# Kernel optimization log

Hardware: AMD Instinct MI355X
Metric: run time of the kernel (lower is better)

## Reference

```python
import jax, jax.numpy as jnp
import numpy as np

GROUP_SIZE = 16
MIN_SIGMA = 1e-4


def setup_inputs() -> dict:
    key = jax.random.key(0)
    k1, k2, k3 = jax.random.split(key, 3)
    B, N, M, F = 4, 8192, 4096, 64
    return {
        "point_cloud": jax.random.normal(k1, (B, 3, N), dtype=jnp.float32),
        "query_cloud": jax.random.normal(k2, (B, 3, M), dtype=jnp.float32),
        "point_features": jax.random.normal(k3, (B, F, N), dtype=jnp.float32),
        "temperature": jnp.asarray(1.0, dtype=jnp.float32),
    }


def reference(point_cloud, query_cloud, point_features, temperature):
    # point_cloud: (B,3,N), query_cloud: (B,3,M), point_features: (B,F,N)
    k = GROUP_SIZE
    # Pairwise squared distances (B, M, N): ||q||^2 + ||p||^2 - 2 q.p
    q_sq = jnp.sum(query_cloud ** 2, axis=1)              # (B, M)
    p_sq = jnp.sum(point_cloud ** 2, axis=1)              # (B, N)
    qp = jnp.einsum('bdm,bdn->bmn', query_cloud, point_cloud)
    d2 = q_sq[:, :, None] + p_sq[:, None, :] - 2.0 * qp   # (B, M, N)
    # k nearest neighbors per query
    _, idx = jax.lax.top_k(-d2, k)                         # (B, M, k)

    # Gather neighbor coords and features: (B, 3, M, k), (B, F, M, k)
    idx_b = idx[:, None, :, :]                             # (B,1,M,k)
    grouped_points = jnp.take_along_axis(
        point_cloud[:, :, None, :], jnp.broadcast_to(idx_b, (idx.shape[0], 3, idx.shape[1], k)), axis=3)
    grouped_features = jnp.take_along_axis(
        point_features[:, :, None, :],
        jnp.broadcast_to(idx_b, (idx.shape[0], point_features.shape[1], idx.shape[1], k)), axis=3)

    # Soft-projection weights
    sigma = jnp.maximum(temperature ** 2, jnp.asarray(MIN_SIGMA, dtype=temperature.dtype))
    deltas = grouped_points - query_cloud[:, :, :, None]   # (B,3,M,k)
    dist = jnp.sum(deltas ** 2, axis=1, keepdims=True) / sigma  # (B,1,M,k)
    weights = jax.nn.softmax(-dist, axis=3)                # (B,1,M,k)

    projected_points = jnp.sum(grouped_points * weights, axis=3)     # (B,3,M)
    propagated_features = jnp.sum(grouped_features * weights, axis=3)  # (B,F,M)
    return (projected_points, propagated_features)
```

## Files before the change

kernel.cpp:

```cpp
#include <hip/hip_runtime.h>


#define BB 4
#define NN 8192
#define MM 4096
#define FF 64
#define KK 16
#define CHUNK 2048
#define NCHUNK 4
#define QPW 8
#define QPB 64
#define SCAP 54
#define NTHR 1024

__global__ __launch_bounds__(256) void transpose_feat(const float* __restrict__ pf,
                                                      float* __restrict__ pfT) {
    __shared__ float tile[64][65];
    const int b = blockIdx.y;
    const int n0 = blockIdx.x * 64;
    const int t = threadIdx.x;
    const int n = t & 63, fq = t >> 6;
#pragma unroll
    for (int i = 0; i < 16; ++i) {
        int f = fq * 16 + i;
        tile[f][n] = pf[(size_t)b * FF * NN + (size_t)f * NN + n0 + n];
    }
    __syncthreads();
    const int f2 = t & 63, nq = t >> 6;
#pragma unroll
    for (int i = 0; i < 16; ++i) {
        int nn2 = nq * 16 + i;
        pfT[(size_t)b * NN * FF + (size_t)(n0 + nn2) * FF + f2] = tile[f2][nn2];
    }
}

__device__ __forceinline__ unsigned mapf(float f) {
    unsigned u = __float_as_uint(f);
    return (u & 0x80000000u) ? ~u : (u | 0x80000000u);
}
__device__ __forceinline__ float unmapf(unsigned k) {
    return (k & 0x80000000u) ? __uint_as_float(k ^ 0x80000000u)
                             : __uint_as_float(~k);
}

#define STAGE(C)                                                            \
    do {                                                                    \
        if (t < CHUNK / 4) {                                                \
            int base_ = (C)*CHUNK + t * 4;                                  \
            float4 x4_ = *(const float4*)(pcb + base_);                     \
            float4 y4_ = *(const float4*)(pcb + NN + base_);                \
            float4 z4_ = *(const float4*)(pcb + 2 * NN + base_);            \
            *(float4*)(s_pts + t * 4) = x4_;                                \
            *(float4*)(s_pts + CHUNK + t * 4) = y4_;                        \
            *(float4*)(s_pts + 2 * CHUNK + t * 4) = z4_;                    \
            float4 p4_;                                                     \
            p4_.x = fmaf(x4_.x, x4_.x, fmaf(y4_.x, y4_.x, z4_.x * z4_.x));  \
            p4_.y = fmaf(x4_.y, x4_.y, fmaf(y4_.y, y4_.y, z4_.y * z4_.y));  \
            p4_.z = fmaf(x4_.z, x4_.z, fmaf(y4_.z, y4_.z, z4_.z * z4_.z));  \
            p4_.w = fmaf(x4_.w, x4_.w, fmaf(y4_.w, y4_.w, z4_.w * z4_.w));  \
            *(float4*)(s_pts + 3 * CHUNK + t * 4) = p4_;                    \
        }                                                                   \
    } while (0)

#define VAL(X, Y, Z, PS, Q) \
    fmaf((X), qx2[Q], fmaf((Y), qy2[Q], fmaf((Z), qz2[Q], (PS))))

#define PUSH(WQ, V, I)                                          \
    do {                                                        \
        int pos_ = atomicAdd(&s_cnt[WQ], 1);                    \
        if (pos_ < SCAP) {                                      \
            s_surv[((WQ)*SCAP + pos_) * 2] = (V);               \
            s_surv[((WQ)*SCAP + pos_) * 2 + 1] = __int_as_float(I); \
        }                                                       \
    } while (0)

__global__ __launch_bounds__(NTHR, 4) void soft_proj_kernel(
    const float* __restrict__ pc, const float* __restrict__ qc,
    const float* __restrict__ pf, const float* __restrict__ pfT,
    const float* __restrict__ temp, float* __restrict__ out, int useT) {
    __shared__ __align__(16) float s_pts[4 * CHUNK];
    __shared__ __align__(16) float s_surv[QPB * SCAP * 2];
    __shared__ int s_cnt[QPB];
    __shared__ int s_sel[QPB * KK];
    __shared__ float s_thr[2 * QPB];

    const int bid = blockIdx.x;
    const int b = bid >> 6;
    const int m0 = (bid & 63) * QPB;
    const int t = threadIdx.x;
    const int wave = t >> 6;
    const int lane = t & 63;
    const int pairIdx = wave & 7;
    const int half = wave >> 3;

    const float* pcb = pc + (size_t)b * 3 * NN;
    const float* qcb = qc + (size_t)b * 3 * MM;

    float qx2[QPW], qy2[QPW], qz2[QPW];
#pragma unroll
    for (int q = 0; q < QPW; ++q) {
        int m = m0 + pairIdx * QPW + q;
        qx2[q] = -2.0f * qcb[m];
        qy2[q] = -2.0f * qcb[MM + m];
        qz2[q] = -2.0f * qcb[2 * MM + m];
    }

    float mn[QPW];
#pragma unroll
    for (int q = 0; q < QPW; ++q) mn[q] = 3.0e38f;

    for (int c = 0; c < NCHUNK; ++c) {
        __syncthreads();
        STAGE(c);
        __syncthreads();
        const int ob = half * 1024 + lane * 4;
#pragma unroll
        for (int g = 0; g < 4; ++g) {
            int oo = ob + g * 256;
            float4 x4 = *(const float4*)(s_pts + oo);
            float4 y4 = *(const float4*)(s_pts + CHUNK + oo);
            float4 z4 = *(const float4*)(s_pts + 2 * CHUNK + oo);
            float4 p4 = *(const float4*)(s_pts + 3 * CHUNK + oo);
#pragma unroll
            for (int q = 0; q < QPW; ++q) {
                float v0 = VAL(x4.x, y4.x, z4.x, p4.x, q);
                float v1 = VAL(x4.y, y4.y, z4.y, p4.y, q);
                float v2 = VAL(x4.z, y4.z, z4.z, p4.z, q);
                float v3 = VAL(x4.w, y4.w, z4.w, p4.w, q);
                mn[q] = fminf(mn[q], fminf(fminf(v0, v1), fminf(v2, v3)));
            }
        }
    }

    float thrv[QPW];
#pragma unroll
    for (int q = 0; q < QPW; ++q) {
        unsigned key = mapf(mn[q]);
        unsigned res = 0u;
        for (int bb = 31; bb >= 8; --bb) {
            unsigned cand = res | (1u << bb);
            unsigned long long bal = __ballot(key < cand);
            int c2 = __popcll(bal);
            if (c2 < 8) res = cand;
        }
        thrv[q] = unmapf(res | 0xFFu);
    }
    if (lane == 0) {
#pragma unroll
        for (int q = 0; q < QPW; ++q)
            s_thr[half * QPB + pairIdx * QPW + q] = thrv[q];
    }
    if (t < QPB) s_cnt[t] = 0;
    __syncthreads();
#pragma unroll
    for (int q = 0; q < QPW; ++q)
        thrv[q] = fmaxf(s_thr[pairIdx * QPW + q], s_thr[QPB + pairIdx * QPW + q]);

    for (int c = 0; c < NCHUNK; ++c) {
        __syncthreads();
        STAGE(c);
        __syncthreads();
        const int ob = half * 1024 + lane * 4;
#pragma unroll
        for (int g = 0; g < 4; ++g) {
            int oo = ob + g * 256;
            float4 x4 = *(const float4*)(s_pts + oo);
            float4 y4 = *(const float4*)(s_pts + CHUNK + oo);
            float4 z4 = *(const float4*)(s_pts + 2 * CHUNK + oo);
            float4 p4 = *(const float4*)(s_pts + 3 * CHUNK + oo);
            int gi = c * CHUNK + oo;
#pragma unroll
            for (int q = 0; q < QPW; ++q) {
                int wqq = pairIdx * QPW + q;
                float v0 = VAL(x4.x, y4.x, z4.x, p4.x, q);
                float v1 = VAL(x4.y, y4.y, z4.y, p4.y, q);
                float v2 = VAL(x4.z, y4.z, z4.z, p4.z, q);
                float v3 = VAL(x4.w, y4.w, z4.w, p4.w, q);
                if (v0 <= thrv[q]) PUSH(wqq, v0, gi + 0);
                if (v1 <= thrv[q]) PUSH(wqq, v1, gi + 1);
                if (v2 <= thrv[q]) PUSH(wqq, v2, gi + 2);
                if (v3 <= thrv[q]) PUSH(wqq, v3, gi + 3);
            }
        }
    }
    __syncthreads();

#pragma unroll
    for (int qq = 0; qq < 4; ++qq) {
        int wq = wave * 4 + qq;
        int cnt = s_cnt[wq];
        cnt = __builtin_amdgcn_readfirstlane(cnt);
        if (cnt > SCAP) cnt = SCAP;
        bool valid = lane < cnt;
        float mv = 0.f;
        int mi = 0;
        if (valid) {
            mv = s_surv[(wq * SCAP + lane) * 2];
            mi = __float_as_int(s_surv[(wq * SCAP + lane) * 2 + 1]);
        }
        int rank = 0;
        for (int j = 0; j < cnt; ++j) {
            float vj = s_surv[(wq * SCAP + j) * 2];
            int ij = __float_as_int(s_surv[(wq * SCAP + j) * 2 + 1]);
            if (valid && (vj < mv || (vj == mv && ij < mi))) rank++;
        }
        if (valid && rank < KK) s_sel[wq * KK + rank] = mi;
    }
    __syncthreads();

    float* stage = s_surv;
    float tval = temp[0];
    float sigma = fmaxf(tval * tval, 1.0e-4f);
    float inv_sigma = 1.0f / sigma;
    const float* pfTb = pfT + (size_t)b * NN * FF;
    const float* pfb = pf + (size_t)b * FF * NN;

#pragma unroll
    for (int qq = 0; qq < 4; ++qq) {
        int wq = wave * 4 + qq;
        int m = m0 + wq;
        float qxe = qcb[m], qye = qcb[MM + m], qze = qcb[2 * MM + m];
        int ik[KK];
        float dk[KK];
#pragma unroll
        for (int k = 0; k < KK; ++k) {
            int ii = __builtin_amdgcn_readfirstlane(s_sel[wq * KK + k]);
            ik[k] = ii;
            float px = pcb[ii], py = pcb[NN + ii], pz = pcb[2 * NN + ii];
            float dx = px - qxe, dy = py - qye, dz = pz - qze;
            dk[k] = fmaf(dx, dx, fmaf(dy, dy, dz * dz));
        }
        float dmin = dk[0];
#pragma unroll
        for (int k = 1; k < KK; ++k) dmin = fminf(dmin, dk[k]);
        float ssum = 0.f, facc = 0.f, sx = 0.f, sy = 0.f, sz = 0.f;
#pragma unroll
        for (int k = 0; k < KK; ++k) {
            float e = __expf((dmin - dk[k]) * inv_sigma);
            ssum += e;
            float px = pcb[ik[k]], py = pcb[NN + ik[k]], pz = pcb[2 * NN + ik[k]];
            sx = fmaf(e, px, sx);
            sy = fmaf(e, py, sy);
            sz = fmaf(e, pz, sz);
            float fv = useT ? pfTb[(size_t)ik[k] * FF + lane]
                            : pfb[(size_t)lane * NN + ik[k]];
            facc = fmaf(e, fv, facc);
        }
        float rs = 1.0f / ssum;
        stage[lane * 65 + wq] = facc * rs;
        if (lane == 0) {
            stage[64 * 65 + wq] = sx * rs;
            stage[65 * 65 + wq] = sy * rs;
            stage[66 * 65 + wq] = sz * rs;
        }
    }
    __syncthreads();

    const size_t featOff = (size_t)BB * 3 * MM;
    for (int j = t; j < 67 * 64; j += NTHR) {
        int row = j >> 6, col = j & 63;
        float v = stage[row * 65 + col];
        int m = m0 + col;
        if (row < 64)
            out[featOff + (size_t)b * FF * MM + (size_t)row * MM + m] = v;
        else
            out[(size_t)b * 3 * MM + (size_t)(row - 64) * MM + m] = v;
    }
}

extern "C" void kernel_launch(void* const* d_in, const int* in_sizes, int n_in,
                              void* d_out, int out_size, void* d_ws, size_t ws_size,
                              hipStream_t stream) {
    (void)in_sizes; (void)n_in; (void)out_size;
    const float* pc = (const float*)d_in[0];
    const float* qc = (const float*)d_in[1];
    const float* pf = (const float*)d_in[2];
    const float* temp = (const float*)d_in[3];
    float* out = (float*)d_out;
    float* pfT = (float*)d_ws;
    const size_t needT = (size_t)BB * NN * FF * sizeof(float);
    int useT = (ws_size >= needT && d_ws != nullptr) ? 1 : 0;

    if (useT) {
        hipLaunchKernelGGL(transpose_feat, dim3(NN / 64, BB), dim3(256), 0, stream,
                           pf, pfT);
    }
    hipLaunchKernelGGL(soft_proj_kernel, dim3((BB * MM) / QPB), dim3(NTHR), 0,
                       stream, pc, qc, pf, pfT, temp, out, useT);
}
```

Before: 131.9 us.

## Shrink blocks, double-buffer point staging, use packed FMA, vectorize transpose

```diff
diff --git a/kernel.cpp b/kernel.cpp
--- a/kernel.cpp
+++ b/kernel.cpp
@@ -6,12 +6,26 @@
 #define MM 4096
 #define FF 64
 #define KK 16
-#define CHUNK 2048
-#define NCHUNK 4
+#define CHUNK 1024
+#define NCHUNK 8
 #define QPW 8
-#define QPB 64
-#define SCAP 54
-#define NTHR 1024
+#define QPB 16
+#define SCAP 52
+#define NTHR 256
+#define WAVES 4
+
+typedef float f32x2 __attribute__((ext_vector_type(2)));
+
+__device__ __forceinline__ f32x2 pkfma(f32x2 a, f32x2 b, f32x2 c) {
+#if __has_builtin(__builtin_elementwise_fma)
+    return __builtin_elementwise_fma(a, b, c);
+#else
+    f32x2 r;
+    r.x = fmaf(a.x, b.x, c.x);
+    r.y = fmaf(a.y, b.y, c.y);
+    return r;
+#endif
+}
 
 __global__ __launch_bounds__(256) void transpose_feat(const float* __restrict__ pf,
                                                       float* __restrict__ pfT) {
@@ -19,18 +33,30 @@
     const int b = blockIdx.y;
     const int n0 = blockIdx.x * 64;
     const int t = threadIdx.x;
-    const int n = t & 63, fq = t >> 6;
-#pragma unroll
-    for (int i = 0; i < 16; ++i) {
-        int f = fq * 16 + i;
-        tile[f][n] = pf[(size_t)b * FF * NN + (size_t)f * NN + n0 + n];
-    }
-    __syncthreads();
-    const int f2 = t & 63, nq = t >> 6;
-#pragma unroll
-    for (int i = 0; i < 16; ++i) {
-        int nn2 = nq * 16 + i;
-        pfT[(size_t)b * NN * FF + (size_t)(n0 + nn2) * FF + f2] = tile[f2][nn2];
+    const int nq = t & 15;
+    const int r0 = t >> 4;
+#pragma unroll
+    for (int i = 0; i < 4; ++i) {
+        int f = r0 + i * 16;
+        float4 v = *(const float4*)(pf + (size_t)b * FF * NN + (size_t)f * NN +
+                                    n0 + nq * 4);
+        tile[f][nq * 4 + 0] = v.x;
+        tile[f][nq * 4 + 1] = v.y;
+        tile[f][nq * 4 + 2] = v.z;
+        tile[f][nq * 4 + 3] = v.w;
+    }
+    __syncthreads();
+    const int f4 = (t & 15) * 4;
+    const int nr = t >> 4;
+#pragma unroll
+    for (int i = 0; i < 4; ++i) {
+        int n = nr + i * 16;
+        float4 v;
+        v.x = tile[f4 + 0][n];
+        v.y = tile[f4 + 1][n];
+        v.z = tile[f4 + 2][n];
+        v.w = tile[f4 + 3][n];
+        *(float4*)(pfT + (size_t)b * NN * FF + (size_t)(n0 + n) * FF + f4) = v;
     }
 }
 
@@ -43,93 +69,104 @@
                              : __uint_as_float(~k);
 }
 
-#define STAGE(C)                                                            \
-    do {                                                                    \
-        if (t < CHUNK / 4) {                                                \
-            int base_ = (C)*CHUNK + t * 4;                                  \
-            float4 x4_ = *(const float4*)(pcb + base_);                     \
-            float4 y4_ = *(const float4*)(pcb + NN + base_);                \
-            float4 z4_ = *(const float4*)(pcb + 2 * NN + base_);            \
-            *(float4*)(s_pts + t * 4) = x4_;                                \
-            *(float4*)(s_pts + CHUNK + t * 4) = y4_;                        \
-            *(float4*)(s_pts + 2 * CHUNK + t * 4) = z4_;                    \
-            float4 p4_;                                                     \
-            p4_.x = fmaf(x4_.x, x4_.x, fmaf(y4_.x, y4_.x, z4_.x * z4_.x));  \
-            p4_.y = fmaf(x4_.y, x4_.y, fmaf(y4_.y, y4_.y, z4_.y * z4_.y));  \
-            p4_.z = fmaf(x4_.z, x4_.z, fmaf(y4_.z, y4_.z, z4_.z * z4_.z));  \
-            p4_.w = fmaf(x4_.w, x4_.w, fmaf(y4_.w, y4_.w, z4_.w * z4_.w));  \
-            *(float4*)(s_pts + 3 * CHUNK + t * 4) = p4_;                    \
-        }                                                                   \
+#define LOADREG(C)                                   \
+    do {                                             \
+        int base_ = (C)*CHUNK + t * 4;               \
+        rx = *(const float4*)(pcb + base_);          \
+        ry = *(const float4*)(pcb + NN + base_);     \
+        rz = *(const float4*)(pcb + 2 * NN + base_); \
     } while (0)
 
-#define VAL(X, Y, Z, PS, Q) \
-    fmaf((X), qx2[Q], fmaf((Y), qy2[Q], fmaf((Z), qz2[Q], (PS))))
-
-#define PUSH(WQ, V, I)                                          \
-    do {                                                        \
-        int pos_ = atomicAdd(&s_cnt[WQ], 1);                    \
-        if (pos_ < SCAP) {                                      \
-            s_surv[((WQ)*SCAP + pos_) * 2] = (V);               \
+#define WRITELDS(P)                                                   \
+    do {                                                              \
+        int i_ = t * 4;                                               \
+        float4 p4_;                                                   \
+        p4_.x = fmaf(rx.x, rx.x, fmaf(ry.x, ry.x, rz.x * rz.x));      \
+        p4_.y = fmaf(rx.y, rx.y, fmaf(ry.y, ry.y, rz.y * rz.y));      \
+        p4_.z = fmaf(rx.z, rx.z, fmaf(ry.z, ry.z, rz.z * rz.z));      \
+        p4_.w = fmaf(rx.w, rx.w, fmaf(ry.w, ry.w, rz.w * rz.w));      \
+        *(float4*)(&s_pts[P][0][i_]) = rx;                            \
+        *(float4*)(&s_pts[P][1][i_]) = ry;                            \
+        *(float4*)(&s_pts[P][2][i_]) = rz;                            \
+        *(float4*)(&s_pts[P][3][i_]) = p4_;                           \
+    } while (0)
+
+#define PUSH(WQ, V, I)                                              \
+    do {                                                            \
+        int pos_ = atomicAdd(&s_cnt[WQ], 1);                        \
+        if (pos_ < SCAP) {                                          \
+            s_surv[((WQ)*SCAP + pos_) * 2] = (V);                   \
             s_surv[((WQ)*SCAP + pos_) * 2 + 1] = __int_as_float(I); \
-        }                                                       \
+        }                                                           \
     } while (0)
 
 __global__ __launch_bounds__(NTHR, 4) void soft_proj_kernel(
     const float* __restrict__ pc, const float* __restrict__ qc,
     const float* __restrict__ pf, const float* __restrict__ pfT,
     const float* __restrict__ temp, float* __restrict__ out, int useT) {
-    __shared__ __align__(16) float s_pts[4 * CHUNK];
+    __shared__ __align__(16) float s_pts[2][4][CHUNK];
     __shared__ __align__(16) float s_surv[QPB * SCAP * 2];
     __shared__ int s_cnt[QPB];
     __shared__ int s_sel[QPB * KK];
     __shared__ float s_thr[2 * QPB];
 
     const int bid = blockIdx.x;
-    const int b = bid >> 6;
-    const int m0 = (bid & 63) * QPB;
+    const int b = bid >> 8;
+    const int m0 = (bid & 255) * QPB;
     const int t = threadIdx.x;
     const int wave = t >> 6;
     const int lane = t & 63;
-    const int pairIdx = wave & 7;
-    const int half = wave >> 3;
+    const int pairIdx = wave & 1;
+    const int half = wave >> 1;
 
     const float* pcb = pc + (size_t)b * 3 * NN;
     const float* qcb = qc + (size_t)b * 3 * MM;
 
-    float qx2[QPW], qy2[QPW], qz2[QPW];
+    f32x2 qx2[QPW], qy2[QPW], qz2[QPW];
 #pragma unroll
     for (int q = 0; q < QPW; ++q) {
         int m = m0 + pairIdx * QPW + q;
-        qx2[q] = -2.0f * qcb[m];
-        qy2[q] = -2.0f * qcb[MM + m];
-        qz2[q] = -2.0f * qcb[2 * MM + m];
-    }
-
+        float vx = -2.0f * qcb[m];
+        float vy = -2.0f * qcb[MM + m];
+        float vz = -2.0f * qcb[2 * MM + m];
+        qx2[q].x = vx; qx2[q].y = vx;
+        qy2[q].x = vy; qy2[q].y = vy;
+        qz2[q].x = vz; qz2[q].y = vz;
+    }
+
+    float4 rx, ry, rz;
     float mn[QPW];
 #pragma unroll
     for (int q = 0; q < QPW; ++q) mn[q] = 3.0e38f;
 
+    LOADREG(0);
+    WRITELDS(0);
+    __syncthreads();
     for (int c = 0; c < NCHUNK; ++c) {
+        const int p = c & 1;
+        if (c + 1 < NCHUNK) LOADREG(c + 1);
+        const int ob = half * 512 + lane * 4;
+#pragma unroll
+        for (int g = 0; g < 2; ++g) {
+            int oo = ob + g * 256;
+            float4 x4 = *(const float4*)(&s_pts[p][0][oo]);
+            float4 y4 = *(const float4*)(&s_pts[p][1][oo]);
+            float4 z4 = *(const float4*)(&s_pts[p][2][oo]);
+            float4 p4 = *(const float4*)(&s_pts[p][3][oo]);
+            f32x2 x01 = {x4.x, x4.y}, x23 = {x4.z, x4.w};
+            f32x2 y01 = {y4.x, y4.y}, y23 = {y4.z, y4.w};
+            f32x2 z01 = {z4.x, z4.y}, z23 = {z4.z, z4.w};
+            f32x2 s01 = {p4.x, p4.y}, s23 = {p4.z, p4.w};
+#pragma unroll
+            for (int q = 0; q < QPW; ++q) {
+                f32x2 v01 = pkfma(x01, qx2[q], pkfma(y01, qy2[q], pkfma(z01, qz2[q], s01)));
+                f32x2 v23 = pkfma(x23, qx2[q], pkfma(y23, qy2[q], pkfma(z23, qz2[q], s23)));
+                mn[q] = fminf(mn[q],
+                              fminf(fminf(v01.x, v01.y), fminf(v23.x, v23.y)));
+            }
+        }
+        if (c + 1 < NCHUNK) WRITELDS(p ^ 1);
         __syncthreads();
-        STAGE(c);
-        __syncthreads();
-        const int ob = half * 1024 + lane * 4;
-#pragma unroll
-        for (int g = 0; g < 4; ++g) {
-            int oo = ob + g * 256;
-            float4 x4 = *(const float4*)(s_pts + oo);
-            float4 y4 = *(const float4*)(s_pts + CHUNK + oo);
-            float4 z4 = *(const float4*)(s_pts + 2 * CHUNK + oo);
-            float4 p4 = *(const float4*)(s_pts + 3 * CHUNK + oo);
-#pragma unroll
-            for (int q = 0; q < QPW; ++q) {
-                float v0 = VAL(x4.x, y4.x, z4.x, p4.x, q);
-                float v1 = VAL(x4.y, y4.y, z4.y, p4.y, q);
-                float v2 = VAL(x4.z, y4.z, z4.z, p4.z, q);
-                float v3 = VAL(x4.w, y4.w, z4.w, p4.w, q);
-                mn[q] = fminf(mn[q], fminf(fminf(v0, v1), fminf(v2, v3)));
-            }
-        }
     }
 
     float thrv[QPW];
@@ -156,40 +193,45 @@
     for (int q = 0; q < QPW; ++q)
         thrv[q] = fmaxf(s_thr[pairIdx * QPW + q], s_thr[QPB + pairIdx * QPW + q]);
 
+    LOADREG(0);
+    WRITELDS(0);
+    __syncthreads();
     for (int c = 0; c < NCHUNK; ++c) {
-        __syncthreads();
-        STAGE(c);
-        __syncthreads();
-        const int ob = half * 1024 + lane * 4;
-#pragma unroll
-        for (int g = 0; g < 4; ++g) {
+        const int p = c & 1;
+        if (c + 1 < NCHUNK) LOADREG(c + 1);
+        const int ob = half * 512 + lane * 4;
+#pragma unroll
+        for (int g = 0; g < 2; ++g) {
             int oo = ob + g * 256;
-            float4 x4 = *(const float4*)(s_pts + oo);
-            float4 y4 = *(const float4*)(s_pts + CHUNK + oo);
-            float4 z4 = *(const float4*)(s_pts + 2 * CHUNK + oo);
-            float4 p4 = *(const float4*)(s_pts + 3 * CHUNK + oo);
+            float4 x4 = *(const float4*)(&s_pts[p][0][oo]);
+            float4 y4 = *(const float4*)(&s_pts[p][1][oo]);
+            float4 z4 = *(const float4*)(&s_pts[p][2][oo]);
+            float4 p4 = *(const float4*)(&s_pts[p][3][oo]);
+            f32x2 x01 = {x4.x, x4.y}, x23 = {x4.z, x4.w};
+            f32x2 y01 = {y4.x, y4.y}, y23 = {y4.z, y4.w};
+            f32x2 z01 = {z4.x, z4.y}, z23 = {z4.z, z4.w};
+            f32x2 s01 = {p4.x, p4.y}, s23 = {p4.z, p4.w};
             int gi = c * CHUNK + oo;
 #pragma unroll
             for (int q = 0; q < QPW; ++q) {
                 int wqq = pairIdx * QPW + q;
-                float v0 = VAL(x4.x, y4.x, z4.x, p4.x, q);
-                float v1 = VAL(x4.y, y4.y, z4.y, p4.y, q);
-                float v2 = VAL(x4.z, y4.z, z4.z, p4.z, q);
-                float v3 = VAL(x4.w, y4.w, z4.w, p4.w, q);
-                if (v0 <= thrv[q]) PUSH(wqq, v0, gi + 0);
-                if (v1 <= thrv[q]) PUSH(wqq, v1, gi + 1);
-                if (v2 <= thrv[q]) PUSH(wqq, v2, gi + 2);
-                if (v3 <= thrv[q]) PUSH(wqq, v3, gi + 3);
+                f32x2 v01 = pkfma(x01, qx2[q], pkfma(y01, qy2[q], pkfma(z01, qz2[q], s01)));
+                f32x2 v23 = pkfma(x23, qx2[q], pkfma(y23, qy2[q], pkfma(z23, qz2[q], s23)));
+                if (v01.x <= thrv[q]) PUSH(wqq, v01.x, gi + 0);
+                if (v01.y <= thrv[q]) PUSH(wqq, v01.y, gi + 1);
+                if (v23.x <= thrv[q]) PUSH(wqq, v23.x, gi + 2);
+                if (v23.y <= thrv[q]) PUSH(wqq, v23.y, gi + 3);
             }
         }
+        if (c + 1 < NCHUNK) WRITELDS(p ^ 1);
+        __syncthreads();
     }
     __syncthreads();
 
 #pragma unroll
     for (int qq = 0; qq < 4; ++qq) {
         int wq = wave * 4 + qq;
-        int cnt = s_cnt[wq];
-        cnt = __builtin_amdgcn_readfirstlane(cnt);
+        int cnt = __builtin_amdgcn_readfirstlane(s_cnt[wq]);
         if (cnt > SCAP) cnt = SCAP;
         bool valid = lane < cnt;
         float mv = 0.f;
@@ -247,19 +289,19 @@
             facc = fmaf(e, fv, facc);
         }
         float rs = 1.0f / ssum;
-        stage[lane * 65 + wq] = facc * rs;
+        stage[lane * 17 + wq] = facc * rs;
         if (lane == 0) {
-            stage[64 * 65 + wq] = sx * rs;
-            stage[65 * 65 + wq] = sy * rs;
-            stage[66 * 65 + wq] = sz * rs;
+            stage[64 * 17 + wq] = sx * rs;
+            stage[65 * 17 + wq] = sy * rs;
+            stage[66 * 17 + wq] = sz * rs;
         }
     }
     __syncthreads();
 
     const size_t featOff = (size_t)BB * 3 * MM;
-    for (int j = t; j < 67 * 64; j += NTHR) {
-        int row = j >> 6, col = j & 63;
-        float v = stage[row * 65 + col];
+    for (int j = t; j < 67 * QPB; j += NTHR) {
+        int row = j >> 4, col = j & 15;
+        float v = stage[row * 17 + col];
         int m = m0 + col;
         if (row < 64)
             out[featOff + (size_t)b * FF * MM + (size_t)row * MM + m] = v;
```

Result: no change. 132.7 us (+0.6%).
